# Kernel tuning notes

Hardware: AMD Instinct MI355X
Metric: run time of the kernel (lower is better)

## Reference

```python
import jax, jax.numpy as jnp
import numpy as np

N, E = 50000, 800000
D_IN, D_DEG, D_MSG, D_UP, D_H = 128, 16, 128, 128, 256
D = D_IN + D_DEG          # 144, node feature after degree-tag concat
MSG_IN = 2 * D            # 288
UPD_IN = D + D_MSG        # 272

def _mlp_params(key, d_in, d_h, d_out):
    k1, k2 = jax.random.split(key)
    s1 = 1.0 / np.sqrt(d_in)
    s2 = 1.0 / np.sqrt(d_h)
    return (jax.random.uniform(k1, (d_in, d_h), jnp.float32, -s1, s1),
            jnp.zeros((d_h,), jnp.float32),
            jax.random.uniform(k2, (d_h, d_out), jnp.float32, -s2, s2),
            jnp.zeros((d_out,), jnp.float32))

def setup_inputs() -> dict:
    key = jax.random.key(0)
    kx, ke, kd, km, ku = jax.random.split(key, 5)
    x = jax.random.normal(kx, (N, D_IN), jnp.float32)
    edge_index = jax.random.randint(ke, (2, E), 0, N, jnp.int64)
    degrees = jax.random.uniform(kd, (N, D_DEG), jnp.float32)
    mW1, mb1, mW2, mb2 = _mlp_params(km, MSG_IN, D_H, D_MSG)
    uW1, ub1, uW2, ub2 = _mlp_params(ku, UPD_IN, D_H, D_UP)
    return {"x": x, "edge_index": edge_index, "degrees": degrees,
            "msg_W1": mW1, "msg_b1": mb1, "msg_W2": mW2, "msg_b2": mb2,
            "upd_W1": uW1, "upd_b1": ub1, "upd_W2": uW2, "upd_b2": ub2}

def _mlp(h, W1, b1, W2, b2):
    return jax.nn.relu(h @ W1 + b1) @ W2 + b2

def reference(x, edge_index, degrees,
              msg_W1, msg_b1, msg_W2, msg_b2,
              upd_W1, upd_b1, upd_W2, upd_b2):
    # degree_as_tag + retain_features -> concat node features with degree tags
    h = jnp.concatenate([x, degrees], axis=-1)          # [N, D]
    # flow='source_to_target': i = edge_index[1] (target), j = edge_index[0] (source)
    src, tgt = edge_index[0], edge_index[1]
    h_i = h[tgt]                                        # [E, D]
    h_j = h[src]                                        # [E, D]
    msgs = _mlp(jnp.concatenate([h_i, h_j], axis=-1),   # [E, 2D] -> [E, D_MSG]
                msg_W1, msg_b1, msg_W2, msg_b2)
    # sparse sum over source dim == scatter-add onto targets
    agg = jax.ops.segment_sum(msgs, tgt, num_segments=N)  # [N, D_MSG]
    out = _mlp(jnp.concatenate([h, agg], axis=-1),
               upd_W1, upd_b1, upd_W2, upd_b2)          # [N, D_UP]
    return out
```

## Files before the change

kernel.cpp:

```cpp
#include <hip/hip_runtime.h>


#define N_NODES 50000
#define E_EDGES 800000
#define DF   144
#define DIN  128
#define DDEG 16
#define DMSG 128
#define SA_LD 296
#define SH_LD 264
#define PQ_LD 512
#define KA_LD 168
#define EP_W  68
#define NSLOT 50176
#define CAP8  16
#define OVER_CAP 4096
#define PQ_BLOCKS 782
#define HIST_BLOCKS 3125
#define PREP_BLOCKS 3516
#define PACK_BLOCKS 108

typedef __attribute__((ext_vector_type(8))) short short8;
typedef __attribute__((ext_vector_type(4))) float floatx4;
typedef __attribute__((ext_vector_type(4))) unsigned int uintx4;

__device__ __forceinline__ unsigned int fasu(float f){
  union { float f; unsigned int u; } v; v.f = f; return v.u;
}
__device__ __forceinline__ float uasf(unsigned int u){
  union { unsigned int u; float f; } v; v.u = u; return v.f;
}
__device__ __forceinline__ short f2bf(float f){
  unsigned int i = fasu(f);
  unsigned int r = i + 0x7fffu + ((i >> 16) & 1u);
  return (short)(r >> 16);
}
__device__ __forceinline__ unsigned int pk_trunc(float lo, float hi){
  return __builtin_amdgcn_perm(fasu(hi), fasu(lo), 0x07060302u);
}

__global__ void sentinel_kernel(float* __restrict__ out){
  int i = blockIdx.x * blockDim.x + threadIdx.x;
  if (i < N_NODES * DMSG){ out[i] = 2.0f; }
}

__device__ __forceinline__ void pack_w_dev(const float* __restrict__ W,
                                           short* __restrict__ Wp,
                                           int Ksrc, int nT, int t){
  int lane = t & 63;
  int rest = t >> 6;
  int nt = rest % nT;
  int chunk = rest / nT;
  int Ncols = nT * 16;
  int n = nt * 16 + (lane & 15);
  int kbase = chunk * 32 + (lane >> 4) * 8;
  short8 v;
  for (int j = 0; j < 8; ++j){
    int k = kbase + j;
    short o = 0;
    if (k < Ksrc){ o = f2bf(W[(size_t)k * Ncols + n]); }
    v[j] = o;
  }
  *(short8*)(Wp + (size_t)t * 8) = v;
}
__device__ __forceinline__ void pack_w1pq_dev(const float* __restrict__ W1,
                                              short* __restrict__ Wp, int t){
  int lane = t & 63;
  int rest = t >> 6;
  int nt = rest % 32;
  int chunk = rest / 32;
  int col = nt * 16 + (lane & 15);
  int kbase = chunk * 32 + (lane >> 4) * 8;
  short8 v;
  for (int j = 0; j < 8; ++j){
    int k = kbase + j;
    short o = 0;
    if (k < 144){
      float w = (col < 256) ? W1[(size_t)k * 256 + col]
                            : W1[(size_t)(144 + k) * 256 + (col - 256)];
      o = f2bf(w);
    }
    v[j] = o;
  }
  *(short8*)(Wp + (size_t)t * 8) = v;
}

__global__ void prep_pack_kernel(const float* __restrict__ x, const float* __restrict__ deg,
                                 const float* __restrict__ mW1, const float* __restrict__ mW2,
                                 const float* __restrict__ uW1, const float* __restrict__ uW2,
                                 short* __restrict__ w1pq, short* __restrict__ w2m,
                                 short* __restrict__ w1u, short* __restrict__ w2u,
                                 int* __restrict__ cnt8, int* __restrict__ nOver,
                                 short* __restrict__ h){
  if (blockIdx.x >= PREP_BLOCKS){
    int t2 = (blockIdx.x - PREP_BLOCKS) * 256 + threadIdx.x;
    if (t2 < 4096){ pack_w_dev(mW2, w2m, 256, 8, t2); }
    else if (t2 < 13312){ pack_w_dev(uW1, w1u, 272, 16, t2 - 4096); }
    else if (t2 < 17408){ pack_w_dev(uW2, w2u, 256, 8, t2 - 13312); }
    else { pack_w1pq_dev(mW1, w1pq, t2 - 17408); }
    return;
  }
  int i = blockIdx.x * 256 + threadIdx.x;
  if (i < 8 * NSLOT){ cnt8[i] = 0; }
  if (i == 0){ *nOver = 0; }
  if (i < N_NODES * 18){
    int n = i / 18;
    int j = i - n * 18;
    const float* src;
    if (j < 16){ src = x + (size_t)n * DIN + (size_t)j * 8; }
    else       { src = deg + (size_t)n * DDEG + (size_t)(j - 16) * 8; }
    short8 v;
    for (int t = 0; t < 8; ++t){ v[t] = f2bf(src[t]); }
    *(short8*)(h + (size_t)n * DF + (size_t)j * 8) = v;
  }
}

__launch_bounds__(256, 2)
__global__ void pq_scatter_kernel(const short* __restrict__ h, const short* __restrict__ w1pq,
                                  const float* __restrict__ b1, short* __restrict__ PQ,
                                  const int* __restrict__ ei, int* __restrict__ cnt8,
                                  int* __restrict__ nOver, unsigned int* __restrict__ over,
                                  unsigned short* __restrict__ es8){
  __shared__ __align__(16) unsigned int sE[4 * 32 * EP_W];

  const int g = blockIdx.x;
  const bool isG = ((g % 5) == 0) && ((g / 5) < PQ_BLOCKS);
  if (!isG){
    unsigned int xcd;
    asm("s_getreg_b32 %0, hwreg(HW_REG_XCC_ID, 0, 32)" : "=s"(xcd));
    xcd &= 7u;
    int nb = (g / 5) + 1; if (nb > PQ_BLOCKS) nb = PQ_BLOCKS;
    int e = (g - nb) * 256 + threadIdx.x;
    if (e < E_EDGES){
      int s = ei[e];
      int t = ei[E_EDGES + e];
      if ((unsigned)s >= (unsigned)N_NODES) s = 0;
      if ((unsigned)t >= (unsigned)N_NODES) t = 0;
      int* cp = cnt8 + (size_t)xcd * NSLOT + t;
      int r = __hip_atomic_fetch_add(cp, 1, __ATOMIC_RELAXED, __HIP_MEMORY_SCOPE_WORKGROUP);
      if (r < CAP8){
        es8[((size_t)xcd * N_NODES + t) * CAP8 + r] = (unsigned short)s;
      } else {
        int p = atomicAdd(nOver, 1);
        if (p < OVER_CAP){ over[p] = ((unsigned int)t << 16) | (unsigned int)s; }
      }
    }
    return;
  }

  const int tid  = threadIdx.x;
  const int lane = tid & 63;
  const int wave = tid >> 6;
  const int q    = lane >> 4;
  const int lr   = lane & 15;
  const int n0   = (g / 5) * 64;
  short* sA = (short*)sE;

  {
    int row = tid >> 2;
    int quarter = tid & 3;
    int n = n0 + row;
    if (n >= N_NODES) n = 0;
    const short* hp = h + (size_t)n * DF;
    short* dstp = sA + row * KA_LD + quarter * 40;
    #pragma unroll
    for (int c5 = 0; c5 < 5; ++c5){
      int col = quarter * 40 + c5 * 8;
      short8 v;
      if (col < DF){
        v = *(const short8*)(hp + col);
      } else {
        for (int j = 0; j < 8; ++j){ v[j] = 0; }
      }
      *(short8*)(dstp + c5 * 8) = v;
    }
  }
  __syncthreads();

  floatx4 acc[4][8];
  #pragma unroll
  for (int it = 0; it < 4; ++it){
    #pragma unroll
    for (int jt = 0; jt < 8; ++jt){
      #pragma unroll
      for (int r = 0; r < 4; ++r){ acc[it][jt][r] = 0.0f; }
    }
  }

  for (int kc = 0; kc < 5; ++kc){
    short8 aF[4];
    #pragma unroll
    for (int it = 0; it < 4; ++it){
      aF[it] = *(const short8*)(sA + (it * 16 + lr) * KA_LD + kc * 32 + q * 8);
    }
    #pragma unroll
    for (int jt = 0; jt < 8; ++jt){
      short8 bF = *(const short8*)(w1pq + ((size_t)(kc * 32 + wave * 8 + jt) * 64 + lane) * 8);
      #pragma unroll
      for (int it = 0; it < 4; ++it){
        acc[it][jt] = __builtin_amdgcn_mfma_f32_16x16x32_bf16(aF[it], bF, acc[it][jt], 0, 0, 0);
      }
    }
  }
  __syncthreads();

  const int waveBase = wave * (32 * EP_W);
  #pragma unroll
  for (int rnd = 0; rnd < 2; ++rnd){
    #pragma unroll
    for (int il = 0; il < 2; ++il){
      const int it = rnd * 2 + il;
      #pragma unroll
      for (int jt = 0; jt < 8; ++jt){
        int col  = (wave * 8 + jt) * 16 + lr;
        float bb = (col < 256) ? b1[col] : 0.0f;
        floatx4 a = acc[it][jt];
        unsigned int pk01 = pk_trunc(a[0] + bb, a[1] + bb);
        unsigned int pk23 = pk_trunc(a[2] + bb, a[3] + bb);
        unsigned int send = (lr & 1) ? pk01 : pk23;
        unsigned int t = (unsigned int)__shfl_xor((int)send, 1, 64);
        int lrow;
        unsigned int w0, w1;
        if ((lr & 1) == 0){
          lrow = il * 16 + q * 4;
          w0 = (pk01 & 0xffffu) | ((t & 0xffffu) << 16);
          w1 = (pk01 >> 16)     | (t & 0xffff0000u);
        } else {
          lrow = il * 16 + q * 4 + 2;
          w0 = (t & 0xffffu) | ((pk23 & 0xffffu) << 16);
          w1 = (t >> 16)     | (pk23 & 0xffff0000u);
        }
        int wv = jt * 8 + (lr >> 1);
        sE[waveBase + lrow * EP_W + wv] = w0;
        sE[waveBase + (lrow + 1) * EP_W + wv] = w1;
      }
    }
    #pragma unroll
    for (int rr = 0; rr < 8; ++rr){
      int lrow = rr * 4 + (lane >> 4);
      int grow = n0 + rnd * 32 + lrow;
      uintx4 v = *(const uintx4*)(sE + waveBase + lrow * EP_W + (lane & 15) * 4);
      if (grow < N_NODES){
        *(uintx4*)((unsigned int*)PQ + (size_t)grow * 256 + wave * 64 + (lane & 15) * 4) = v;
      }
    }
  }
}

__launch_bounds__(256, 8)
__global__ void hsum_kernel(const short* __restrict__ PQ, const unsigned short* __restrict__ es8,
                            const int* __restrict__ cnt8, const unsigned int* __restrict__ over,
                            const int* __restrict__ nOver, short* __restrict__ HsumB,
                            int* __restrict__ dtot){
  const int lane = threadIdx.x & 63;
  const int wave = threadIdx.x >> 6;
  const int t = blockIdx.x * 4 + wave;
  const unsigned int* PQu = (const unsigned int*)PQ;

  uint2 pv = *(const uint2*)(PQu + (size_t)t * 256 + lane * 2);
  int craw = (lane < 8) ? cnt8[(size_t)lane * NSLOT + t] : 0;
  int cc = craw < CAP8 ? craw : CAP8;

  int c0 = __shfl(cc, 0, 64), c1 = __shfl(cc, 1, 64), c2 = __shfl(cc, 2, 64), c3 = __shfl(cc, 3, 64);
  int c4 = __shfl(cc, 4, 64), c5 = __shfl(cc, 5, 64), c6 = __shfl(cc, 6, 64), c7 = __shfl(cc, 7, 64);
  int dtrue = __shfl(craw, 0, 64) + __shfl(craw, 1, 64) + __shfl(craw, 2, 64) + __shfl(craw, 3, 64)
            + __shfl(craw, 4, 64) + __shfl(craw, 5, 64) + __shfl(craw, 6, 64) + __shfl(craw, 7, 64);
  int e1 = c0, e2 = e1 + c1, e3 = e2 + c2, e4 = e3 + c3;
  int e5 = e4 + c4, e6 = e5 + c5, e7 = e6 + c6, e8 = e7 + c7;
  if (lane == 0){ dtot[t] = dtrue; }

  float a0 = 0.0f, a1 = 0.0f, a2 = 0.0f, a3 = 0.0f;
  float Pf0 = uasf(pv.x << 16), Pf1 = uasf(pv.x & 0xffff0000u);
  float Pf2 = uasf(pv.y << 16), Pf3 = uasf(pv.y & 0xffff0000u);

  #define LDQ(idx) (*(const uint2*)(PQu + (size_t)(unsigned int)__shfl((int)el, (idx), 64) * 256 + 128 + lane * 2))
  #define ACCQ(qv) { float v;                                        \
      v = Pf0 + uasf((qv).x << 16);          a0 += v > 0.0f ? v : 0.0f; \
      v = Pf1 + uasf((qv).x & 0xffff0000u);  a1 += v > 0.0f ? v : 0.0f; \
      v = Pf2 + uasf((qv).y << 16);          a2 += v > 0.0f ? v : 0.0f; \
      v = Pf3 + uasf((qv).y & 0xffff0000u);  a3 += v > 0.0f ? v : 0.0f; }

  for (int base = 0; base < e8; base += 64){
    int m = e8 - base; if (m > 64) m = 64;
    int jj = base + lane;
    int f1 = jj >= e1, f2 = jj >= e2, f3 = jj >= e3, f4 = jj >= e4;
    int f5 = jj >= e5, f6 = jj >= e6, f7 = jj >= e7;
    int x  = f1 + f2 + f3 + f4 + f5 + f6 + f7;
    int ex = (f1 ? c0 : 0) + (f2 ? c1 : 0) + (f3 ? c2 : 0) + (f4 ? c3 : 0)
           + (f5 ? c4 : 0) + (f6 ? c5 : 0) + (f7 ? c6 : 0);
    unsigned int el = (jj < e8)
        ? (unsigned int)es8[((size_t)x * N_NODES + t) * CAP8 + (jj - ex)] : 0u;
    uint2 q0 = LDQ(0);
    uint2 q1 = LDQ(1);
    uint2 q2 = LDQ(2);
    uint2 q3 = LDQ(3);
    for (int j = 0; j < m; j += 4){
      uint2 t0 = q0, t1 = q1, t2 = q2, t3 = q3;
      int i0 = j + 4, i1 = j + 5, i2 = j + 6, i3 = j + 7;
      q0 = LDQ(i0 < 64 ? i0 : 0);
      q1 = LDQ(i1 < 64 ? i1 : 0);
      q2 = LDQ(i2 < 64 ? i2 : 0);
      q3 = LDQ(i3 < 64 ? i3 : 0);
      ACCQ(t0);
      if (j + 1 < m){ ACCQ(t1); }
      if (j + 2 < m){ ACCQ(t2); }
      if (j + 3 < m){ ACCQ(t3); }
    }
  }

  if (dtrue > e8){
    int no = *nOver;
    if (no > OVER_CAP) no = OVER_CAP;
    for (int p = 0; p < no; ++p){
      unsigned int w = over[p];
      if ((int)(w >> 16) == t){
        unsigned int s1 = w & 0xffffu;
        uint2 qv = *(const uint2*)(PQu + (size_t)s1 * 256 + 128 + lane * 2);
        ACCQ(qv);
      }
    }
  }
  #undef ACCQ
  #undef LDQ

  uint2 o;
  o.x = pk_trunc(a0, a1);
  o.y = pk_trunc(a2, a3);
  *(uint2*)((unsigned int*)HsumB + (size_t)t * 128 + lane * 2) = o;
}

__launch_bounds__(256, 4)
__global__ void node2_kernel(const short* __restrict__ h, const short* __restrict__ HsumB,
                             const int* __restrict__ dtot,
                             const short* __restrict__ w2m, const float* __restrict__ b2m,
                             const short* __restrict__ w1u, const float* __restrict__ b1u,
                             const short* __restrict__ w2u, const float* __restrict__ b2u,
                             float* __restrict__ out){
  __shared__ __align__(16) short sBuf[64 * SA_LD];
  __shared__ int sCnt[64];
  const int tid  = threadIdx.x;
  const int lane = tid & 63;
  const int wave = tid >> 6;
  const int q    = lane >> 4;
  const int lr   = lane & 15;
  const int n0   = blockIdx.x * 64;

  {
    int row = tid >> 2;
    int qtr = tid & 3;
    int n = n0 + row; if (n >= N_NODES) n = 0;
    const short* hp = HsumB + (size_t)n * 256 + qtr * 64;
    short* dst = sBuf + row * SA_LD + qtr * 64;
    #pragma unroll
    for (int c = 0; c < 8; ++c){
      *(short8*)(dst + c * 8) = *(const short8*)(hp + c * 8);
    }
    if (tid < 64){
      int n2 = n0 + tid; if (n2 >= N_NODES) n2 = 0;
      sCnt[tid] = dtot[n2];
    }
  }
  __syncthreads();

  floatx4 agga[4][2];
  #pragma unroll
  for (int it = 0; it < 4; ++it){
    #pragma unroll
    for (int jt = 0; jt < 2; ++jt){
      #pragma unroll
      for (int r = 0; r < 4; ++r){ agga[it][jt][r] = 0.0f; }
    }
  }
  for (int kc = 0; kc < 8; ++kc){
    short8 aF[4];
    #pragma unroll
    for (int it = 0; it < 4; ++it){
      aF[it] = *(const short8*)(sBuf + (it * 16 + lr) * SA_LD + kc * 32 + q * 8);
    }
    #pragma unroll
    for (int jt = 0; jt < 2; ++jt){
      short8 bF = *(const short8*)(w2m + ((size_t)(kc * 8 + wave * 2 + jt) * 64 + lane) * 8);
      #pragma unroll
      for (int it = 0; it < 4; ++it){
        agga[it][jt] = __builtin_amdgcn_mfma_f32_16x16x32_bf16(aF[it], bF, agga[it][jt], 0, 0, 0);
      }
    }
  }
  __syncthreads();

  if (tid < 128){
    int row = tid >> 1;
    int half = tid & 1;
    int n = n0 + row; if (n >= N_NODES) n = 0;
    const short* srcp = h + (size_t)n * DF + half * 72;
    short* dstp = sBuf + row * SA_LD + half * 72;
    #pragma unroll
    for (int c = 0; c < 9; ++c){
      *(short8*)(dstp + c * 8) = *(const short8*)(srcp + c * 8);
    }
  } else {
    int t2 = tid - 128;
    int row = t2 >> 1;
    int half = t2 & 1;
    short* padp = sBuf + row * SA_LD + 272 + half * 8;
    #pragma unroll
    for (int t = 0; t < 8; ++t){ padp[t] = 0; }
  }
  #pragma unroll
  for (int jt = 0; jt < 2; ++jt){
    int colm = wave * 32 + jt * 16 + lr;
    int colb = 144 + wave * 32 + jt * 16 + (lr & ~1);
    float bb = b2m[colm];
    #pragma unroll
    for (int it = 0; it < 4; ++it){
      int rb = it * 16 + q * 4;
      float v0 = agga[it][jt][0] + (float)sCnt[rb + 0] * bb;
      float v1 = agga[it][jt][1] + (float)sCnt[rb + 1] * bb;
      float v2 = agga[it][jt][2] + (float)sCnt[rb + 2] * bb;
      float v3 = agga[it][jt][3] + (float)sCnt[rb + 3] * bb;
      unsigned int pk01 = pk_trunc(v0, v1);
      unsigned int pk23 = pk_trunc(v2, v3);
      unsigned int send = (lr & 1) ? pk01 : pk23;
      unsigned int t = (unsigned int)__shfl_xor((int)send, 1, 64);
      int row0;
      unsigned int w0, w1;
      if ((lr & 1) == 0){
        row0 = rb;
        w0 = (pk01 & 0xffffu) | ((t & 0xffffu) << 16);
        w1 = (pk01 >> 16)     | (t & 0xffff0000u);
      } else {
        row0 = rb + 2;
        w0 = (t & 0xffffu) | ((pk23 & 0xffffu) << 16);
        w1 = (t >> 16)     | (pk23 & 0xffff0000u);
      }
      *(unsigned int*)(sBuf + row0 * SA_LD + colb) = w0;
      *(unsigned int*)(sBuf + (row0 + 1) * SA_LD + colb) = w1;
    }
  }
  __syncthreads();

  floatx4 acc[4][4];
  #pragma unroll
  for (int it = 0; it < 4; ++it){
    #pragma unroll
    for (int jt = 0; jt < 4; ++jt){
      #pragma unroll
      for (int r = 0; r < 4; ++r){ acc[it][jt][r] = 0.0f; }
    }
  }
  for (int kc = 0; kc < 9; ++kc){
    short8 aF[4];
    #pragma unroll
    for (int it = 0; it < 4; ++it){
      aF[it] = *(const short8*)(sBuf + (it * 16 + lr) * SA_LD + kc * 32 + q * 8);
    }
    #pragma unroll
    for (int jt = 0; jt < 4; ++jt){
      short8 bF = *(const short8*)(w1u + ((size_t)(kc * 16 + wave * 4 + jt) * 64 + lane) * 8);
      #pragma unroll
      for (int it = 0; it < 4; ++it){
        acc[it][jt] = __builtin_amdgcn_mfma_f32_16x16x32_bf16(aF[it], bF, acc[it][jt], 0, 0, 0);
      }
    }
  }
  __syncthreads();
  #pragma unroll
  for (int jt = 0; jt < 4; ++jt){
    int col  = wave * 64 + jt * 16 + lr;
    int colb = wave * 64 + jt * 16 + (lr & ~1);
    float bb = b1u[col];
    #pragma unroll
    for (int it = 0; it < 4; ++it){
      floatx4 a = acc[it][jt];
      float v0 = a[0] + bb; v0 = v0 > 0.0f ? v0 : 0.0f;
      float v1 = a[1] + bb; v1 = v1 > 0.0f ? v1 : 0.0f;
      float v2 = a[2] + bb; v2 = v2 > 0.0f ? v2 : 0.0f;
      float v3 = a[3] + bb; v3 = v3 > 0.0f ? v3 : 0.0f;
      unsigned int pk01 = pk_trunc(v0, v1);
      unsigned int pk23 = pk_trunc(v2, v3);
      unsigned int send = (lr & 1) ? pk01 : pk23;
      unsigned int t = (unsigned int)__shfl_xor((int)send, 1, 64);
      int row0;
      unsigned int w0, w1;
      if ((lr & 1) == 0){
        row0 = it * 16 + q * 4;
        w0 = (pk01 & 0xffffu) | ((t & 0xffffu) << 16);
        w1 = (pk01 >> 16)     | (t & 0xffff0000u);
      } else {
        row0 = it * 16 + q * 4 + 2;
        w0 = (t & 0xffffu) | ((pk23 & 0xffffu) << 16);
        w1 = (t >> 16)     | (pk23 & 0xffff0000u);
      }
      *(unsigned int*)(sBuf + row0 * SH_LD + colb) = w0;
      *(unsigned int*)(sBuf + (row0 + 1) * SH_LD + colb) = w1;
    }
  }
  __syncthreads();

  floatx4 acc2[4][2];
  #pragma unroll
  for (int it = 0; it < 4; ++it){
    #pragma unroll
    for (int jt = 0; jt < 2; ++jt){
      #pragma unroll
      for (int r = 0; r < 4; ++r){ acc2[it][jt][r] = 0.0f; }
    }
  }
  for (int kc = 0; kc < 8; ++kc){
    short8 aF[4];
    #pragma unroll
    for (int it = 0; it < 4; ++it){
      aF[it] = *(const short8*)(sBuf + (it * 16 + lr) * SH_LD + kc * 32 + q * 8);
    }
    #pragma unroll
    for (int jt = 0; jt < 2; ++jt){
      short8 bF = *(const short8*)(w2u + ((size_t)(kc * 8 + wave * 2 + jt) * 64 + lane) * 8);
      #pragma unroll
      for (int it = 0; it < 4; ++it){
        acc2[it][jt] = __builtin_amdgcn_mfma_f32_16x16x32_bf16(aF[it], bF, acc2[it][jt], 0, 0, 0);
      }
    }
  }
  __syncthreads();
  float* sO = (float*)sBuf;
  #pragma unroll
  for (int jt = 0; jt < 2; ++jt){
    int col = wave * 32 + jt * 16 + lr;
    float bb = b2u[col];
    #pragma unroll
    for (int it = 0; it < 4; ++it){
      #pragma unroll
      for (int r = 0; r < 4; ++r){
        sO[(it * 16 + q * 4 + r) * 132 + col] = acc2[it][jt][r] + bb;
      }
    }
  }
  __syncthreads();
  #pragma unroll
  for (int rr = 0; rr < 8; ++rr){
    int row = rr * 8 + (tid >> 5);
    int n = n0 + row;
    if (n < N_NODES){
      *(floatx4*)(out + (size_t)n * DMSG + (tid & 31) * 4) =
          *(const floatx4*)(sO + row * 132 + (tid & 31) * 4);
    }
  }
}

extern "C" void kernel_launch(void* const* d_in, const int* in_sizes, int n_in,
                              void* d_out, int out_size, void* d_ws, size_t ws_size,
                              hipStream_t stream){
  const float* x   = (const float*)d_in[0];
  const int*   ei  = (const int*)d_in[1];
  const float* deg = (const float*)d_in[2];
  const float* mW1 = (const float*)d_in[3];
  const float* mb1 = (const float*)d_in[4];
  const float* mW2 = (const float*)d_in[5];
  const float* mb2 = (const float*)d_in[6];
  const float* uW1 = (const float*)d_in[7];
  const float* ub1 = (const float*)d_in[8];
  const float* uW2 = (const float*)d_in[9];
  const float* ub2 = (const float*)d_in[10];

  char* ws = (char*)d_ws;
  size_t off = 0;
  short* HsumB = (short*)(ws + off); off += (size_t)N_NODES * 256 * 2;
  short* hbuf  = (short*)(ws + off); off += (size_t)N_NODES * DF * 2;
  off = (off + 255) & ~(size_t)255;
  short* w2m  = (short*)(ws + off); off += (size_t)8 * 8 * 64 * 8 * 2;
  short* w1u  = (short*)(ws + off); off += (size_t)9 * 16 * 64 * 8 * 2;
  short* w2u  = (short*)(ws + off); off += (size_t)8 * 8 * 64 * 8 * 2;
  short* w1pq = (short*)(ws + off); off += (size_t)5 * 32 * 64 * 8 * 2;
  off = (off + 255) & ~(size_t)255;
  short* PQ = (short*)(ws + off); off += (size_t)N_NODES * PQ_LD * 2;
  unsigned short* es8 = (unsigned short*)(ws + off);
  off += (size_t)8 * N_NODES * CAP8 * 2;
  off = (off + 255) & ~(size_t)255;
  int* cnt8 = (int*)(ws + off); off += (size_t)8 * NSLOT * 4;
  int* dtot = (int*)(ws + off); off += (size_t)NSLOT * 4;
  int* nOver = (int*)(ws + off); off += 256;
  unsigned int* over = (unsigned int*)(ws + off); off += (size_t)OVER_CAP * 4;

  if (ws_size < off){
    sentinel_kernel<<<(N_NODES * DMSG + 255) / 256, 256, 0, stream>>>((float*)d_out);
    return;
  }

  prep_pack_kernel<<<PREP_BLOCKS + PACK_BLOCKS, 256, 0, stream>>>(
      x, deg, mW1, mW2, uW1, uW2, w1pq, w2m, w1u, w2u, cnt8, nOver, hbuf);
  pq_scatter_kernel<<<PQ_BLOCKS + HIST_BLOCKS, 256, 0, stream>>>(
      hbuf, w1pq, mb1, PQ, ei, cnt8, nOver, over, es8);
  hsum_kernel<<<(N_NODES + 3) / 4, 256, 0, stream>>>(PQ, es8, cnt8, over, nOver, HsumB, dtot);
  node2_kernel<<<(N_NODES + 63) / 64, 256, 0, stream>>>(hbuf, HsumB, dtot, w2m, mb2,
                                                        w1u, ub1, w2u, ub2,
                                                        (float*)d_out);
}
```

Measured before the change: 256.0 us.

## Fuse edge-gather hidden-sum kernel into node MLP kernel via shared memory

Merges the per-node gather/ReLU-sum kernel into the node2 MLP kernel. Each of the four waves computes 16 rows of the hidden sum directly into shared memory instead of writing HsumB and dtot to global memory and reading them back. This removes a kernel launch and the global round trip for the intermediate. The cost is far less parallelism for the latency-bound gather: only 782 blocks with each wave looping over 16 nodes serially, at lower occupancy (launch bounds 4 instead of 8).

```diff
diff --git a/kernel.cpp b/kernel.cpp
--- a/kernel.cpp
+++ b/kernel.cpp
@@ -19,6 +19,7 @@
 #define HIST_BLOCKS 3125
 #define PREP_BLOCKS 3516
 #define PACK_BLOCKS 108
+#define N2_BLOCKS 782
 
 typedef __attribute__((ext_vector_type(8))) short short8;
 typedef __attribute__((ext_vector_type(4))) float floatx4;
@@ -247,95 +248,16 @@
   }
 }
 
-__launch_bounds__(256, 8)
-__global__ void hsum_kernel(const short* __restrict__ PQ, const unsigned short* __restrict__ es8,
-                            const int* __restrict__ cnt8, const unsigned int* __restrict__ over,
-                            const int* __restrict__ nOver, short* __restrict__ HsumB,
-                            int* __restrict__ dtot){
-  const int lane = threadIdx.x & 63;
-  const int wave = threadIdx.x >> 6;
-  const int t = blockIdx.x * 4 + wave;
-  const unsigned int* PQu = (const unsigned int*)PQ;
-
-  uint2 pv = *(const uint2*)(PQu + (size_t)t * 256 + lane * 2);
-  int craw = (lane < 8) ? cnt8[(size_t)lane * NSLOT + t] : 0;
-  int cc = craw < CAP8 ? craw : CAP8;
-
-  int c0 = __shfl(cc, 0, 64), c1 = __shfl(cc, 1, 64), c2 = __shfl(cc, 2, 64), c3 = __shfl(cc, 3, 64);
-  int c4 = __shfl(cc, 4, 64), c5 = __shfl(cc, 5, 64), c6 = __shfl(cc, 6, 64), c7 = __shfl(cc, 7, 64);
-  int dtrue = __shfl(craw, 0, 64) + __shfl(craw, 1, 64) + __shfl(craw, 2, 64) + __shfl(craw, 3, 64)
-            + __shfl(craw, 4, 64) + __shfl(craw, 5, 64) + __shfl(craw, 6, 64) + __shfl(craw, 7, 64);
-  int e1 = c0, e2 = e1 + c1, e3 = e2 + c2, e4 = e3 + c3;
-  int e5 = e4 + c4, e6 = e5 + c5, e7 = e6 + c6, e8 = e7 + c7;
-  if (lane == 0){ dtot[t] = dtrue; }
-
-  float a0 = 0.0f, a1 = 0.0f, a2 = 0.0f, a3 = 0.0f;
-  float Pf0 = uasf(pv.x << 16), Pf1 = uasf(pv.x & 0xffff0000u);
-  float Pf2 = uasf(pv.y << 16), Pf3 = uasf(pv.y & 0xffff0000u);
-
-  #define LDQ(idx) (*(const uint2*)(PQu + (size_t)(unsigned int)__shfl((int)el, (idx), 64) * 256 + 128 + lane * 2))
-  #define ACCQ(qv) { float v;                                        \
-      v = Pf0 + uasf((qv).x << 16);          a0 += v > 0.0f ? v : 0.0f; \
-      v = Pf1 + uasf((qv).x & 0xffff0000u);  a1 += v > 0.0f ? v : 0.0f; \
-      v = Pf2 + uasf((qv).y << 16);          a2 += v > 0.0f ? v : 0.0f; \
-      v = Pf3 + uasf((qv).y & 0xffff0000u);  a3 += v > 0.0f ? v : 0.0f; }
-
-  for (int base = 0; base < e8; base += 64){
-    int m = e8 - base; if (m > 64) m = 64;
-    int jj = base + lane;
-    int f1 = jj >= e1, f2 = jj >= e2, f3 = jj >= e3, f4 = jj >= e4;
-    int f5 = jj >= e5, f6 = jj >= e6, f7 = jj >= e7;
-    int x  = f1 + f2 + f3 + f4 + f5 + f6 + f7;
-    int ex = (f1 ? c0 : 0) + (f2 ? c1 : 0) + (f3 ? c2 : 0) + (f4 ? c3 : 0)
-           + (f5 ? c4 : 0) + (f6 ? c5 : 0) + (f7 ? c6 : 0);
-    unsigned int el = (jj < e8)
-        ? (unsigned int)es8[((size_t)x * N_NODES + t) * CAP8 + (jj - ex)] : 0u;
-    uint2 q0 = LDQ(0);
-    uint2 q1 = LDQ(1);
-    uint2 q2 = LDQ(2);
-    uint2 q3 = LDQ(3);
-    for (int j = 0; j < m; j += 4){
-      uint2 t0 = q0, t1 = q1, t2 = q2, t3 = q3;
-      int i0 = j + 4, i1 = j + 5, i2 = j + 6, i3 = j + 7;
-      q0 = LDQ(i0 < 64 ? i0 : 0);
-      q1 = LDQ(i1 < 64 ? i1 : 0);
-      q2 = LDQ(i2 < 64 ? i2 : 0);
-      q3 = LDQ(i3 < 64 ? i3 : 0);
-      ACCQ(t0);
-      if (j + 1 < m){ ACCQ(t1); }
-      if (j + 2 < m){ ACCQ(t2); }
-      if (j + 3 < m){ ACCQ(t3); }
-    }
-  }
-
-  if (dtrue > e8){
-    int no = *nOver;
-    if (no > OVER_CAP) no = OVER_CAP;
-    for (int p = 0; p < no; ++p){
-      unsigned int w = over[p];
-      if ((int)(w >> 16) == t){
-        unsigned int s1 = w & 0xffffu;
-        uint2 qv = *(const uint2*)(PQu + (size_t)s1 * 256 + 128 + lane * 2);
-        ACCQ(qv);
-      }
-    }
-  }
-  #undef ACCQ
-  #undef LDQ
-
-  uint2 o;
-  o.x = pk_trunc(a0, a1);
-  o.y = pk_trunc(a2, a3);
-  *(uint2*)((unsigned int*)HsumB + (size_t)t * 128 + lane * 2) = o;
-}
-
 __launch_bounds__(256, 4)
-__global__ void node2_kernel(const short* __restrict__ h, const short* __restrict__ HsumB,
-                             const int* __restrict__ dtot,
-                             const short* __restrict__ w2m, const float* __restrict__ b2m,
-                             const short* __restrict__ w1u, const float* __restrict__ b1u,
-                             const short* __restrict__ w2u, const float* __restrict__ b2u,
-                             float* __restrict__ out){
+__global__ void hsum_node2_kernel(const short* __restrict__ h, const short* __restrict__ PQ,
+                                  const unsigned short* __restrict__ es8,
+                                  const int* __restrict__ cnt8,
+                                  const unsigned int* __restrict__ over,
+                                  const int* __restrict__ nOver,
+                                  const short* __restrict__ w2m, const float* __restrict__ b2m,
+                                  const short* __restrict__ w1u, const float* __restrict__ b1u,
+                                  const short* __restrict__ w2u, const float* __restrict__ b2u,
+                                  float* __restrict__ out){
   __shared__ __align__(16) short sBuf[64 * SA_LD];
   __shared__ int sCnt[64];
   const int tid  = threadIdx.x;
@@ -344,22 +266,84 @@
   const int q    = lane >> 4;
   const int lr   = lane & 15;
   const int n0   = blockIdx.x * 64;
-
-  {
-    int row = tid >> 2;
-    int qtr = tid & 3;
-    int n = n0 + row; if (n >= N_NODES) n = 0;
-    const short* hp = HsumB + (size_t)n * 256 + qtr * 64;
-    short* dst = sBuf + row * SA_LD + qtr * 64;
-    #pragma unroll
-    for (int c = 0; c < 8; ++c){
-      *(short8*)(dst + c * 8) = *(const short8*)(hp + c * 8);
-    }
-    if (tid < 64){
-      int n2 = n0 + tid; if (n2 >= N_NODES) n2 = 0;
-      sCnt[tid] = dtot[n2];
-    }
-  }
+  const unsigned int* PQu = (const unsigned int*)PQ;
+
+  #define LDQ(idx) (*(const uint2*)(PQu + (size_t)(unsigned int)__shfl((int)el, (idx), 64) * 256 + 128 + lane * 2))
+  #define ACCQ(qv) { float v;                                        \
+      v = Pf0 + uasf((qv).x << 16);          a0 += v > 0.0f ? v : 0.0f; \
+      v = Pf1 + uasf((qv).x & 0xffff0000u);  a1 += v > 0.0f ? v : 0.0f; \
+      v = Pf2 + uasf((qv).y << 16);          a2 += v > 0.0f ? v : 0.0f; \
+      v = Pf3 + uasf((qv).y & 0xffff0000u);  a3 += v > 0.0f ? v : 0.0f; }
+
+  for (int i = 0; i < 16; ++i){
+    const int row = wave * 16 + i;
+    const int t = n0 + row;
+    const int tc = (t < N_NODES) ? t : 0;
+    int craw = (lane < 8) ? cnt8[(size_t)lane * NSLOT + tc] : 0;
+    if (t >= N_NODES){ craw = 0; }
+    int cc = craw < CAP8 ? craw : CAP8;
+    uint2 pv = *(const uint2*)(PQu + (size_t)tc * 256 + lane * 2);
+
+    int c0 = __shfl(cc, 0, 64), c1 = __shfl(cc, 1, 64), c2 = __shfl(cc, 2, 64), c3 = __shfl(cc, 3, 64);
+    int c4 = __shfl(cc, 4, 64), c5 = __shfl(cc, 5, 64), c6 = __shfl(cc, 6, 64), c7 = __shfl(cc, 7, 64);
+    int dtrue = __shfl(craw, 0, 64) + __shfl(craw, 1, 64) + __shfl(craw, 2, 64) + __shfl(craw, 3, 64)
+              + __shfl(craw, 4, 64) + __shfl(craw, 5, 64) + __shfl(craw, 6, 64) + __shfl(craw, 7, 64);
+    int e1 = c0, e2 = e1 + c1, e3 = e2 + c2, e4 = e3 + c3;
+    int e5 = e4 + c4, e6 = e5 + c5, e7 = e6 + c6, e8 = e7 + c7;
+    if (lane == 0){ sCnt[row] = dtrue; }
+
+    float a0 = 0.0f, a1 = 0.0f, a2 = 0.0f, a3 = 0.0f;
+    float Pf0 = uasf(pv.x << 16), Pf1 = uasf(pv.x & 0xffff0000u);
+    float Pf2 = uasf(pv.y << 16), Pf3 = uasf(pv.y & 0xffff0000u);
+
+    for (int base = 0; base < e8; base += 64){
+      int m = e8 - base; if (m > 64) m = 64;
+      int jj = base + lane;
+      int f1 = jj >= e1, f2 = jj >= e2, f3 = jj >= e3, f4 = jj >= e4;
+      int f5 = jj >= e5, f6 = jj >= e6, f7 = jj >= e7;
+      int xb = f1 + f2 + f3 + f4 + f5 + f6 + f7;
+      int ex = (f1 ? c0 : 0) + (f2 ? c1 : 0) + (f3 ? c2 : 0) + (f4 ? c3 : 0)
+             + (f5 ? c4 : 0) + (f6 ? c5 : 0) + (f7 ? c6 : 0);
+      unsigned int el = (jj < e8)
+          ? (unsigned int)es8[((size_t)xb * N_NODES + tc) * CAP8 + (jj - ex)] : 0u;
+      uint2 q0 = LDQ(0);
+      uint2 q1 = LDQ(1);
+      uint2 q2 = LDQ(2);
+      uint2 q3 = LDQ(3);
+      for (int j = 0; j < m; j += 4){
+        uint2 t0 = q0, t1 = q1, t2 = q2, t3 = q3;
+        int i0 = j + 4, i1 = j + 5, i2 = j + 6, i3 = j + 7;
+        q0 = LDQ(i0 < 64 ? i0 : 0);
+        q1 = LDQ(i1 < 64 ? i1 : 0);
+        q2 = LDQ(i2 < 64 ? i2 : 0);
+        q3 = LDQ(i3 < 64 ? i3 : 0);
+        ACCQ(t0);
+        if (j + 1 < m){ ACCQ(t1); }
+        if (j + 2 < m){ ACCQ(t2); }
+        if (j + 3 < m){ ACCQ(t3); }
+      }
+    }
+
+    if (dtrue > e8){
+      int no = *nOver;
+      if (no > OVER_CAP) no = OVER_CAP;
+      for (int p = 0; p < no; ++p){
+        unsigned int w = over[p];
+        if ((int)(w >> 16) == t){
+          unsigned int s1 = w & 0xffffu;
+          uint2 qv = *(const uint2*)(PQu + (size_t)s1 * 256 + 128 + lane * 2);
+          ACCQ(qv);
+        }
+      }
+    }
+
+    uint2 o;
+    o.x = pk_trunc(a0, a1);
+    o.y = pk_trunc(a2, a3);
+    *(uint2*)(sBuf + row * SA_LD + lane * 4) = o;
+  }
+  #undef ACCQ
+  #undef LDQ
   __syncthreads();
 
   floatx4 agga[4][2];
@@ -564,7 +548,6 @@
 
   char* ws = (char*)d_ws;
   size_t off = 0;
-  short* HsumB = (short*)(ws + off); off += (size_t)N_NODES * 256 * 2;
   short* hbuf  = (short*)(ws + off); off += (size_t)N_NODES * DF * 2;
   off = (off + 255) & ~(size_t)255;
   short* w2m  = (short*)(ws + off); off += (size_t)8 * 8 * 64 * 8 * 2;
@@ -577,7 +560,6 @@
   off += (size_t)8 * N_NODES * CAP8 * 2;
   off = (off + 255) & ~(size_t)255;
   int* cnt8 = (int*)(ws + off); off += (size_t)8 * NSLOT * 4;
-  int* dtot = (int*)(ws + off); off += (size_t)NSLOT * 4;
   int* nOver = (int*)(ws + off); off += 256;
   unsigned int* over = (unsigned int*)(ws + off); off += (size_t)OVER_CAP * 4;
 
@@ -590,8 +572,7 @@
       x, deg, mW1, mW2, uW1, uW2, w1pq, w2m, w1u, w2u, cnt8, nOver, hbuf);
   pq_scatter_kernel<<<PQ_BLOCKS + HIST_BLOCKS, 256, 0, stream>>>(
       hbuf, w1pq, mb1, PQ, ei, cnt8, nOver, over, es8);
-  hsum_kernel<<<(N_NODES + 3) / 4, 256, 0, stream>>>(PQ, es8, cnt8, over, nOver, HsumB, dtot);
-  node2_kernel<<<(N_NODES + 63) / 64, 256, 0, stream>>>(hbuf, HsumB, dtot, w2m, mb2,
-                                                        w1u, ub1, w2u, ub2,
-                                                        (float*)d_out);
-}
+  hsum_node2_kernel<<<N2_BLOCKS, 256, 0, stream>>>(
+      hbuf, PQ, es8, cnt8, over, nOver, w2m, mb2, w1u, ub1, w2u, ub2,
+      (float*)d_out);
+}
```

Result: no change. 259.8 us (+1.5%).
